# Performance work log

Hardware: AMD Instinct MI355X
Metric: run time of the kernel (lower is better)

Reference implementation:

```python
import jax, jax.numpy as jnp
import numpy as np

B, N, H = 32, 256, 1024
HEADS, NHID = 8, 128
NCLS = 7
BAND = 24
ALPHA = 0.2          # GAT leaky-relu slope
NEG = -9e15          # masked-attention fill, as in pyGAT


def setup_inputs() -> dict:
    key = jax.random.key(0)
    ks = jax.random.split(key, 16)
    def nrm(k, shp, s=0.02):
        return jax.random.normal(k, shp, dtype=jnp.float32) * s
    hidden_cls = jax.random.normal(ks[0], (B, N, H), dtype=jnp.float32)
    hidden_emo = jax.random.normal(ks[1], (B, N, H), dtype=jnp.float32)
    # causal band cliques, diagonal included (GAT uses clique - eye)
    t = jnp.arange(N)
    band = ((t[None, :] <= t[:, None]) & (t[None, :] > t[:, None] - BAND)).astype(jnp.float32)
    clique = jnp.broadcast_to(band, (B, N, N))
    labels = jax.random.randint(ks[2], (B, N), 0, NCLS)
    pooler_W = nrm(ks[3], (H, H)); pooler_b = jnp.zeros((H,), jnp.float32)
    gat_W = nrm(ks[4], (HEADS, H, NHID))
    gat_a1 = nrm(ks[5], (HEADS, NHID)); gat_a2 = nrm(ks[6], (HEADS, NHID))
    out_W = nrm(ks[7], (H, H))            # heads*nhid == H -> nclass=H
    out_a1 = nrm(ks[8], (H,)); out_a2 = nrm(ks[9], (H,))
    lin1_W = nrm(ks[10], (H, H)); lin1_b = jnp.zeros((H,), jnp.float32)
    lin0_W = nrm(ks[11], (2 * H, H)); lin0_b = jnp.zeros((H,), jnp.float32)
    cls_W = nrm(ks[12], (H, NCLS)); cls_b = jnp.zeros((NCLS,), jnp.float32)
    A = jax.random.uniform(ks[13], (NCLS, NCLS), dtype=jnp.float32) + 0.1
    hmm_A = A / A.sum(axis=1, keepdims=True)   # row-stochastic transition matrix
    return dict(hidden_cls=hidden_cls, hidden_emo=hidden_emo, clique=clique,
                labels=labels, pooler_W=pooler_W, pooler_b=pooler_b,
                gat_W=gat_W, gat_a1=gat_a1, gat_a2=gat_a2,
                out_W=out_W, out_a1=out_a1, out_a2=out_a2,
                lin1_W=lin1_W, lin1_b=lin1_b, lin0_W=lin0_W, lin0_b=lin0_b,
                cls_W=cls_W, cls_b=cls_b, hmm_A=hmm_A)


def _lrelu(x):
    return jnp.where(x > 0, x, ALPHA * x)


def reference(hidden_cls, hidden_emo, clique, labels, pooler_W, pooler_b,
              gat_W, gat_a1, gat_a2, out_W, out_a1, out_a2,
              lin1_W, lin1_b, lin0_W, lin0_b, cls_W, cls_b, hmm_A):
    # PoolerAll: dense + tanh on all token states (dropout = identity in eval)
    fea_cls = jnp.tanh(hidden_cls @ pooler_W + pooler_b)   # [B,N,H] (CLS per utt)
    fea_emo = jnp.tanh(hidden_emo @ pooler_W + pooler_b)   # [B,N,H] (mask tok per utt)

    eyeN = jnp.eye(N, dtype=clique.dtype)
    adjm = (clique - eyeN) > 0                             # [B,N,N] GAT adjacency

    def gat_one(x, am):                                    # x [N,H], am [N,N]
        Wh = jnp.einsum('nf,hfd->hnd', x, gat_W)           # [heads,N,nhid]
        e = _lrelu(jnp.einsum('hnd,hd->hn', Wh, gat_a1)[:, :, None]
                   + jnp.einsum('hnd,hd->hn', Wh, gat_a2)[:, None, :])
        att = jax.nn.softmax(jnp.where(am[None], e, NEG), axis=-1)
        h1 = jax.nn.elu(jnp.einsum('hnm,hmd->hnd', att, Wh))
        h1 = jnp.transpose(h1, (1, 0, 2)).reshape(N, HEADS * NHID)
        Wh2 = h1 @ out_W                                   # out attention layer (concat=False)
        e2 = _lrelu((Wh2 @ out_a1)[:, None] + (Wh2 @ out_a2)[None, :])
        h2 = jax.nn.softmax(jnp.where(am, e2, NEG), axis=-1) @ Wh2
        return jax.nn.elu(h2)                              # [N,H]

    gat_out = jax.vmap(gat_one)(fea_cls, adjm)             # [B,N,H]
    # row 0 replaced by (dropout of) fea_cls row 0, as in the original
    g = jnp.concatenate([fea_cls[:, :1], gat_out[:, 1:]], axis=1)
    g = jnp.concatenate([fea_cls, g @ lin1_W + lin1_b], axis=-1) @ lin0_W + lin0_b
    log_gat = jax.nn.softmax(g @ cls_W + cls_b, axis=-1)   # [B,N,NCLS] (probs)

    # HMM emission probs hmm_B(fea) = softmax(classifier(fea))
    Bprob = jax.nn.softmax(fea_emo @ cls_W + cls_b, axis=-1)  # [B,N,NCLS]
    P0 = jnp.full((NCLS,), 1.0 / NCLS, dtype=jnp.float32)
    AT = hmm_A.T

    def hmm_row(Bp, mrow):                                 # Bp [N,NCLS], mrow [N]
        def step(carry, xs):
            p, started = carry
            bt, m = xs
            p_init = P0 * bt; p_init = p_init / p_init.sum()
            p_tr = (AT @ p) * bt; p_tr = p_tr / p_tr.sum()
            p_new = jnp.where(started, p_tr, p_init)
            valid = m > 0.5
            return (jnp.where(valid, p_new, p), started | valid), None
        (p, _), _ = jax.lax.scan(step, (P0, jnp.asarray(False)), (Bp, mrow))
        return p                                           # final filtered posterior

    log_hmm = jax.vmap(lambda Bp, M: jax.vmap(lambda mr: hmm_row(Bp, mr))(M))(Bprob, clique)

    logits = jnp.log((log_gat + log_hmm) * 0.5).reshape(B * N, NCLS)
    lab = labels.reshape(B * N)
    mask = lab >= 0
    picked = jnp.take_along_axis(logits, jnp.where(mask, lab, 0)[:, None], axis=1)[:, 0]
    loss = -(jnp.where(mask, picked, 0.0).sum() / jnp.maximum(mask.sum(), 1).astype(jnp.float32))
    return loss, logits
```

## Files before the change

kernel.cpp:

```cpp
#include <hip/hip_runtime.h>
#include <hip/hip_bf16.h>
#include <math.h>

typedef __hip_bfloat16 bf16;
typedef __attribute__((ext_vector_type(8))) short short8;
typedef __attribute__((ext_vector_type(4))) float float4v;

static constexpr int Bb = 32, Nn = 256, Hh = 1024, HEADS = 8, NHID = 128, NCLS = 7, BAND = 24;
static constexpr int M = Bb * Nn;
static constexpr float ALPHA = 0.2f;
static constexpr long INEL = (long)M * Hh;

__device__ __forceinline__ float tof(bf16 x) { return __bfloat162float(x); }
__device__ __forceinline__ bf16 tob(float x) { return __float2bfloat16(x); }
__device__ __forceinline__ unsigned short f2bits(float x) {
    bf16 h = __float2bfloat16(x);
    return *(unsigned short*)&h;
}
__device__ __forceinline__ float bits2f(unsigned short u) {
    unsigned v = ((unsigned)u) << 16;
    float f;
    __builtin_memcpy(&f, &v, 4);
    return f;
}

__device__ __forceinline__ void gload16(const void* g, void* l) {
    __builtin_amdgcn_global_load_lds(
        (const __attribute__((address_space(1))) void*)g,
        (__attribute__((address_space(3))) void*)l, 16, 0, 0);
}

static constexpr long OFF_PWT  = 0;
static constexpr long OFF_PB   = 1048576;
static constexpr long OFF_WCT  = 1049600;
static constexpr long OFF_GA1  = 2098176;
static constexpr long OFF_GA2  = 2099200;
static constexpr long OFF_OWT  = 2100224;
static constexpr long OFF_OA1  = 3148800;
static constexpr long OFF_OA2  = 3149824;
static constexpr long OFF_L1WT = 3150848;
static constexpr long OFF_L1B  = 4199424;
static constexpr long OFF_L0WT = 4200448;
static constexpr long OFF_L0B  = 6297600;
static constexpr long OFF_CWT  = 6298624;
static constexpr long OFF_CB   = 6305792;
static constexpr long OFF_HA   = 6305799;
static constexpr long W_TOTAL  = 6305848;

__global__ void probe_k(const void* __restrict__ p, int* __restrict__ flag) {
    int t = threadIdx.x;
    int bad = 0;
    for (int i = t; i < 4096; i += 256) {
        float v = tof(((const bf16*)p)[i]);
        if (!(fabsf(v) < 1e4f)) bad = 1;
    }
    __shared__ int sb[256];
    sb[t] = bad; __syncthreads();
    for (int s = 128; s; s >>= 1) { if (t < s) sb[t] |= sb[t + s]; __syncthreads(); }
    if (t == 0) *flag = sb[0] ? 0 : 1;
}

__device__ __forceinline__ float ldany(const void* p, long i, int isb) {
    return isb ? tof(((const bf16*)p)[i]) : ((const float*)p)[i];
}

__global__ void convert_k(const int* __restrict__ flagp,
                          const void* pW, const void* pb, const void* gW,
                          const void* ga1, const void* ga2, const void* oW,
                          const void* oa1, const void* oa2, const void* l1W,
                          const void* l1b, const void* l0W, const void* l0b,
                          const void* cW, const void* cb, const void* hA,
                          bf16* __restrict__ dst) {
    long idx = (long)blockIdx.x * 256 + threadIdx.x;
    if (idx >= W_TOTAL) return;
    if ((idx >= OFF_L1WT && idx < OFF_L1B) || (idx >= OFF_L0WT && idx < OFF_L0B)) return;
    int isb = *flagp;
    const void* src; long si;
    if      (idx < OFF_PB)   { long l = idx;            long n = l >> 10, k = l & 1023;
                               src = pW;  si = k * 1024 + n; }
    else if (idx < OFF_WCT)  { src = pb;  si = idx - OFF_PB; }
    else if (idx < OFF_GA1)  { long l = idx - OFF_WCT;  long n = l >> 10, f = l & 1023;
                               long h = n >> 7, d = n & 127;
                               src = gW;  si = h * 131072 + f * 128 + d; }
    else if (idx < OFF_GA2)  { src = ga1; si = idx - OFF_GA1; }
    else if (idx < OFF_OWT)  { src = ga2; si = idx - OFF_GA2; }
    else if (idx < OFF_OA1)  { long l = idx - OFF_OWT;  long n = l >> 10, k = l & 1023;
                               src = oW;  si = k * 1024 + n; }
    else if (idx < OFF_OA2)  { src = oa1; si = idx - OFF_OA1; }
    else if (idx < OFF_L1WT) { src = oa2; si = idx - OFF_OA2; }
    else if (idx < OFF_L0WT) { src = l1b; si = idx - OFF_L1B; }
    else if (idx < OFF_CWT)  { src = l0b; si = idx - OFF_L0B; }
    else if (idx < OFF_CB)   { long l = idx - OFF_CWT;  long c = l >> 10, k = l & 1023;
                               src = cW;  si = k * 7 + c; }
    else if (idx < OFF_HA)   { src = cb;  si = idx - OFF_CB; }
    else                     { src = hA;  si = idx - OFF_HA; }
    dst[idx] = tob(ldany(src, si, isb));
}

__global__ void convin_k(const int* __restrict__ flagp, const void* __restrict__ s0,
                         const void* __restrict__ s1, bf16* __restrict__ d0,
                         bf16* __restrict__ d1) {
    const int isb = *flagp;
    if (isb) return;
    long i = ((long)blockIdx.x * 256 + threadIdx.x) * 8;
    const void* s; bf16* d; long off;
    if (i < INEL) { s = s0; d = d0; off = i; }
    else          { s = s1; d = d1; off = i - INEL; }
    const float* f = (const float*)s + off;
    unsigned short tmp[8];
    #pragma unroll
    for (int q = 0; q < 8; ++q) tmp[q] = f2bits(f[q]);
    *(int4*)(d + off) = *(int4*)tmp;
}

__global__ void gvec_k(const int* __restrict__ flagp, const void* __restrict__ l0W,
                       const void* __restrict__ cWr, float* __restrict__ W1T,
                       float* __restrict__ Gb) {
    int k = blockIdx.x;
    int lane = threadIdx.x;
    int isb = *flagp;
    float acc[NCLS];
    #pragma unroll
    for (int c = 0; c < NCLS; ++c) acc[c] = 0.f;
    #pragma unroll
    for (int q = 0; q < 16; ++q) {
        int j = lane * 16 + q;
        float x = ldany(l0W, (long)k * 1024 + j, isb);
        #pragma unroll
        for (int c = 0; c < NCLS; ++c) acc[c] += x * ldany(cWr, (long)j * 7 + c, isb);
    }
    #pragma unroll
    for (int c = 0; c < NCLS; ++c)
        #pragma unroll
        for (int off = 32; off; off >>= 1) acc[c] += __shfl_down(acc[c], off);
    if (lane == 0) {
        #pragma unroll
        for (int c = 0; c < NCLS; ++c) {
            if (k < 1024) W1T[c * 1024 + k] = acc[c];
            else          Gb[(k - 1024) * 7 + c] = acc[c];
        }
    }
}

__global__ void w2_k(const int* __restrict__ flagp, const void* __restrict__ l1W,
                     const float* __restrict__ Gb, float* __restrict__ W2T) {
    int i = blockIdx.x;
    int lane = threadIdx.x;
    int isb = *flagp;
    float acc[NCLS];
    #pragma unroll
    for (int c = 0; c < NCLS; ++c) acc[c] = 0.f;
    #pragma unroll
    for (int q = 0; q < 16; ++q) {
        int o = lane * 16 + q;
        float x = ldany(l1W, (long)i * 1024 + o, isb);
        #pragma unroll
        for (int c = 0; c < NCLS; ++c) acc[c] += x * Gb[o * 7 + c];
    }
    #pragma unroll
    for (int c = 0; c < NCLS; ++c)
        #pragma unroll
        for (int off = 32; off; off >>= 1) acc[c] += __shfl_down(acc[c], off);
    if (lane == 0) {
        #pragma unroll
        for (int c = 0; c < NCLS; ++c) W2T[c * 1024 + i] = acc[c];
    }
}

__global__ void cvec_k(const int* __restrict__ flagp, const void* __restrict__ l1b,
                       const void* __restrict__ l0b, const void* __restrict__ cWr,
                       const void* __restrict__ cbr, const float* __restrict__ Gb,
                       float* __restrict__ cvec) {
    int lane = threadIdx.x;
    int isb = *flagp;
    float acc[NCLS];
    #pragma unroll
    for (int c = 0; c < NCLS; ++c) acc[c] = 0.f;
    for (int o = lane; o < 1024; o += 64) {
        float b1 = ldany(l1b, o, isb);
        float b0 = ldany(l0b, o, isb);
        #pragma unroll
        for (int c = 0; c < NCLS; ++c)
            acc[c] += b1 * Gb[o * 7 + c] + b0 * ldany(cWr, (long)o * 7 + c, isb);
    }
    #pragma unroll
    for (int c = 0; c < NCLS; ++c)
        #pragma unroll
        for (int off = 32; off; off >>= 1) acc[c] += __shfl_down(acc[c], off);
    if (lane == 0) {
        #pragma unroll
        for (int c = 0; c < NCLS; ++c) cvec[c] = acc[c] + ldany(cbr, c, isb);
    }
}

static constexpr int SLOT_US = 256 * 32;

template <int ACT>
__device__ __forceinline__ void gemm_pipe_core(
    const bf16* __restrict__ A0, const bf16* __restrict__ A1, int ksw,
    int strideA, const bf16* __restrict__ Bt, int strideB,
    const bf16* __restrict__ bias, bf16* __restrict__ Cout,
    int Nc, int K, int bm, int bn, unsigned short* lds) {
    const int tid = threadIdx.x;
    const int lane = tid & 63;
    const int wave = tid >> 6;
    const int wm = (wave >> 1) * 64, wn = (wave & 1) * 64;
    const int l15 = lane & 15, quad = lane >> 4;
    const int csw = ((lane & 3) ^ ((lane >> 2) & 3) ^ (lane >> 4)) * 8;
    const int sc8 = (quad ^ (l15 & 3) ^ (l15 >> 2)) * 8;

    long aoff[2], boff[2];
    #pragma unroll
    for (int o = 0; o < 2; ++o) {
        aoff[o] = (long)(bm + wave * 32 + o * 16 + (lane >> 2)) * strideA + csw;
        boff[o] = (long)(bn + wave * 32 + o * 16 + (lane >> 2)) * strideB + csw;
    }
    const int aDst = wave * 32 * 32;
    const int bDst = (128 + wave * 32) * 32;

    const int nt = K / 32;
    float4v acc[4][4];
    #pragma unroll
    for (int i = 0; i < 4; ++i)
        #pragma unroll
        for (int j = 0; j < 4; ++j) acc[i][j] = (float4v){0.f, 0.f, 0.f, 0.f};

    auto stage = [&](int ts, int slot) {
        unsigned short* buf = lds + slot * SLOT_US;
        int ksub = ts * 32;
        const bf16* Ap = A0; int ka = ksub;
        if (ksub >= ksw) { Ap = A1; ka = ksub - ksw; }
        gload16(Ap + aoff[0] + ka, buf + aDst);
        gload16(Ap + aoff[1] + ka, buf + aDst + 512);
        gload16(Bt + boff[0] + ksub, buf + bDst);
        gload16(Bt + boff[1] + ksub, buf + bDst + 512);
    };
    auto frags = [&](int slot, short8* af, short8* bfr) {
        const unsigned short* bufc = lds + slot * SLOT_US;
        #pragma unroll
        for (int i = 0; i < 4; ++i)
            af[i] = *(const short8*)(bufc + (wm + i * 16 + l15) * 32 + sc8);
        #pragma unroll
        for (int j = 0; j < 4; ++j)
            bfr[j] = *(const short8*)(bufc + (128 + wn + j * 16 + l15) * 32 + sc8);
    };

    stage(0, 0); stage(1, 1); stage(2, 2);
    asm volatile("s_waitcnt vmcnt(8)" ::: "memory");
    __builtin_amdgcn_s_barrier();
    asm volatile("" ::: "memory");
    short8 afA[4], bfA[4], afB[4], bfB[4];
    frags(0, afA, bfA);
    int c0 = 0, c1 = 1, c2 = 2;

    for (int t = 0; t < nt; t += 2) {
        asm volatile("s_waitcnt lgkmcnt(0)" ::: "memory");
        if (t < nt - 2) asm volatile("s_waitcnt vmcnt(4)" ::: "memory");
        else            asm volatile("s_waitcnt vmcnt(0)" ::: "memory");
        __builtin_amdgcn_s_barrier();
        asm volatile("" ::: "memory");
        if (t + 3 < nt) stage(t + 3, c0);
        if (t + 1 < nt) frags(c1, afB, bfB);
        __builtin_amdgcn_s_setprio(1);
        #pragma unroll
        for (int i = 0; i < 4; ++i)
            #pragma unroll
            for (int j = 0; j < 4; ++j)
                acc[i][j] = __builtin_amdgcn_mfma_f32_16x16x32_bf16(afA[i], bfA[j], acc[i][j], 0, 0, 0);
        __builtin_amdgcn_s_setprio(0);
        asm volatile("" ::: "memory");
        asm volatile("s_waitcnt lgkmcnt(0)" ::: "memory");
        if (t + 1 < nt - 2) asm volatile("s_waitcnt vmcnt(4)" ::: "memory");
        else                asm volatile("s_waitcnt vmcnt(0)" ::: "memory");
        __builtin_amdgcn_s_barrier();
        asm volatile("" ::: "memory");
        if (t + 4 < nt) stage(t + 4, c1);
        if (t + 2 < nt) frags(c2, afA, bfA);
        __builtin_amdgcn_s_setprio(1);
        #pragma unroll
        for (int i = 0; i < 4; ++i)
            #pragma unroll
            for (int j = 0; j < 4; ++j)
                acc[i][j] = __builtin_amdgcn_mfma_f32_16x16x32_bf16(afB[i], bfB[j], acc[i][j], 0, 0, 0);
        __builtin_amdgcn_s_setprio(0);
        asm volatile("" ::: "memory");
        int n0 = c2, n1 = c0, n2 = c1;
        c0 = n0; c1 = n1; c2 = n2;
    }

    #pragma unroll
    for (int j = 0; j < 4; ++j) {
        int gn = bn + wn + j * 16 + l15;
        float bj = bias ? tof(bias[gn]) : 0.f;
        #pragma unroll
        for (int i = 0; i < 4; ++i) {
            #pragma unroll
            for (int r = 0; r < 4; ++r) {
                int gm = bm + wm + i * 16 + quad * 4 + r;
                float v = acc[i][j][r] + bj;
                if (ACT == 1) v = tanhf(v);
                Cout[(long)gm * Nc + gn] = tob(v);
            }
        }
    }
}

template <int ACT>
__global__ __launch_bounds__(256, 3) void gemm_pipe_k(const bf16* __restrict__ A,
                                                      const bf16* __restrict__ Bt,
                                                      const bf16* __restrict__ bias,
                                                      bf16* __restrict__ Cout,
                                                      int Nc, int K) {
    __shared__ __align__(16) unsigned short lds[3 * SLOT_US];
    gemm_pipe_core<ACT>(A, A, K, K, Bt, K, bias, Cout, Nc, K,
                        blockIdx.x * 128, blockIdx.y * 128, lds);
}

__global__ __launch_bounds__(256, 3) void gemmP_pipe_k(const int* __restrict__ flagp,
                                                       const bf16* __restrict__ rawE,
                                                       const bf16* __restrict__ rawC,
                                                       const bf16* __restrict__ A0,
                                                       const bf16* __restrict__ A1,
                                                       const bf16* __restrict__ Bt,
                                                       const bf16* __restrict__ bias,
                                                       bf16* __restrict__ C0,
                                                       bf16* __restrict__ C1) {
    __shared__ __align__(16) unsigned short lds[3 * SLOT_US];
    const int isb = *flagp;
    const bf16* A = blockIdx.z ? (isb ? rawC : A1) : (isb ? rawE : A0);
    bf16* C = blockIdx.z ? C1 : C0;
    gemm_pipe_core<1>(A, A, Hh, Hh, Bt, Hh, bias, C, Hh, Hh,
                      blockIdx.x * 128, blockIdx.y * 128, lds);
}

__global__ __launch_bounds__(256) void att1f_k(const bf16* __restrict__ Wh,
                                               const bf16* __restrict__ ga1,
                                               const bf16* __restrict__ ga2,
                                               bf16* __restrict__ h1) {
    __shared__ unsigned short S[152][128];
    __shared__ float f1s[152], f2s[152];
    __shared__ float att[128][25];
    const int bx = blockIdx.x;
    const int b = bx >> 4, h = (bx >> 1) & 7, half = bx & 1;
    const int nbase = half * 128;
    const int mstart = half ? (nbase - (BAND - 1)) : 0;
    const int mcount = half ? (256 - mstart) : 128;
    const int t = threadIdx.x;
    const int c = t & 15;

    float av1[8], av2[8];
    {
        union { int4 v; unsigned short us[8]; } u1, u2;
        u1.v = *(const int4*)(ga1 + h * 128 + c * 8);
        u2.v = *(const int4*)(ga2 + h * 128 + c * 8);
        #pragma unroll
        for (int qq = 0; qq < 8; ++qq) { av1[qq] = bits2f(u1.us[qq]); av2[qq] = bits2f(u2.us[qq]); }
    }

    const int iters = (mcount * 16 + 255) >> 8;
    for (int i = 0; i < iters; ++i) {
        int li = i * 256 + t;
        int mr = li >> 4;
        if (mr < mcount) {
            long ga = (long)(b * 256 + mstart + mr) * 1024 + h * 128 + c * 8;
            union { int4 v; unsigned short us[8]; } u;
            u.v = *(const int4*)(Wh + ga);
            float p1 = 0.f, p2 = 0.f;
            #pragma unroll
            for (int qq = 0; qq < 8; ++qq) {
                float f = bits2f(u.us[qq]);
                p1 += f * av1[qq]; p2 += f * av2[qq];
            }
            *(int4*)&S[mr][c * 8] = u.v;
            #pragma unroll
            for (int mask = 1; mask < 16; mask <<= 1) {
                p1 += __shfl_xor(p1, mask);
                p2 += __shfl_xor(p2, mask);
            }
            if (c == 0) { f1s[mr] = p1; f2s[mr] = p2; }
        }
    }
    __syncthreads();

    if (t < 128) {
        int n = nbase + t;
        if (n > 0) {
            int cnt = n < (BAND - 1) ? n : (BAND - 1);
            int m0 = n - cnt;
            float f1n = f1s[n - mstart];
            float e[BAND - 1];
            float mx = -1e30f;
            for (int i = 0; i < cnt; ++i) {
                float v = f1n + f2s[m0 + i - mstart];
                v = v > 0.f ? v : ALPHA * v;
                e[i] = v; mx = fmaxf(mx, v);
            }
            float ss = 0.f;
            for (int i = 0; i < cnt; ++i) { e[i] = __expf(e[i] - mx); ss += e[i]; }
            float inv = 1.0f / ss;
            for (int i = 0; i < cnt; ++i) att[t][i] = e[i] * inv;
        }
    }
    __syncthreads();

    const int wave = t >> 6, lane = t & 63;
    for (int ln = wave; ln < 128; ln += 4) {
        int n = nbase + ln;
        if (n == 0) continue;
        int cnt = n < (BAND - 1) ? n : (BAND - 1);
        int mr0 = n - cnt - mstart;
        float s0 = 0.f, s1 = 0.f;
        for (int i = 0; i < cnt; ++i) {
            float a = att[ln][i];
            unsigned u = *(const unsigned*)&S[mr0 + i][lane * 2];
            s0 += a * bits2f((unsigned short)(u & 0xffff));
            s1 += a * bits2f((unsigned short)(u >> 16));
        }
        s0 = s0 > 0.f ? s0 : expm1f(s0);
        s1 = s1 > 0.f ? s1 : expm1f(s1);
        unsigned out = (unsigned)f2bits(s0) | ((unsigned)f2bits(s1) << 16);
        *(unsigned*)(h1 + (long)(b * 256 + n) * 1024 + h * 128 + lane * 2) = out;
    }
}

__global__ void mean1_k(const bf16* __restrict__ Wh, bf16* __restrict__ h1) {
    int bh = blockIdx.x;
    int h = bh & 7, b = bh >> 3;
    int lane = threadIdx.x;
    float s0 = 0.f, s1 = 0.f;
    long base = (long)(b * 256) * 1024 + h * 128 + lane * 2;
    for (int m = 0; m < 256; ++m) {
        unsigned u = *(const unsigned*)(Wh + base + (long)m * 1024);
        s0 += bits2f((unsigned short)(u & 0xffff));
        s1 += bits2f((unsigned short)(u >> 16));
    }
    s0 *= (1.0f / 256.0f); s1 *= (1.0f / 256.0f);
    s0 = s0 > 0.f ? s0 : expm1f(s0);
    s1 = s1 > 0.f ? s1 : expm1f(s1);
    unsigned out = (unsigned)f2bits(s0) | ((unsigned)f2bits(s1) << 16);
    *(unsigned*)(h1 + base) = out;
}

__global__ void f12b_k(const bf16* __restrict__ Wh2, const bf16* __restrict__ a1,
                       const bf16* __restrict__ a2, float* __restrict__ f1b,
                       float* __restrict__ f2b) {
    int idx = blockIdx.x;
    int lane = threadIdx.x;
    const bf16* row = Wh2 + (long)idx * 1024 + lane * 16;
    float s1 = 0.f, s2 = 0.f;
    #pragma unroll
    for (int half = 0; half < 2; ++half) {
        union { int4 v; unsigned short us[8]; } x, w1, w2;
        x.v  = *(const int4*)(row + half * 8);
        w1.v = *(const int4*)(a1 + lane * 16 + half * 8);
        w2.v = *(const int4*)(a2 + lane * 16 + half * 8);
        #pragma unroll
        for (int q = 0; q < 8; ++q) {
            float f = bits2f(x.us[q]);
            s1 += f * bits2f(w1.us[q]);
            s2 += f * bits2f(w2.us[q]);
        }
    }
    #pragma unroll
    for (int off = 32; off; off >>= 1) {
        s1 += __shfl_down(s1, off);
        s2 += __shfl_down(s2, off);
    }
    if (lane == 0) { f1b[idx] = s1; f2b[idx] = s2; }
}

__global__ __launch_bounds__(256) void att2f_k(const bf16* __restrict__ Wh2,
                                               const float* __restrict__ f1b,
                                               const float* __restrict__ f2b,
                                               bf16* __restrict__ g) {
    __shared__ unsigned short S[152][128];
    __shared__ float att[128][25];
    const int bx = blockIdx.x;
    const int b = bx >> 4, half = (bx >> 3) & 1, jt = bx & 7;
    const int nbase = half * 128;
    const int mstart = half ? (nbase - (BAND - 1)) : 0;
    const int mcount = half ? (256 - mstart) : 128;
    const int t = threadIdx.x;
    const int c = t & 15;

    const int iters = (mcount * 16 + 255) >> 8;
    for (int i = 0; i < iters; ++i) {
        int li = i * 256 + t;
        int mr = li >> 4;
        if (mr < mcount) {
            long ga = (long)(b * 256 + mstart + mr) * 1024 + jt * 128 + c * 8;
            *(int4*)&S[mr][c * 8] = *(const int4*)(Wh2 + ga);
        }
    }
    __syncthreads();

    if (t < 128) {
        int n = nbase + t;
        if (n > 0) {
            int cnt = n < (BAND - 1) ? n : (BAND - 1);
            int m0 = n - cnt;
            float f1n = f1b[b * 256 + n];
            float e[BAND - 1];
            float mx = -1e30f;
            for (int i = 0; i < cnt; ++i) {
                float v = f1n + f2b[b * 256 + m0 + i];
                v = v > 0.f ? v : ALPHA * v;
                e[i] = v; mx = fmaxf(mx, v);
            }
            float ss = 0.f;
            for (int i = 0; i < cnt; ++i) { e[i] = __expf(e[i] - mx); ss += e[i]; }
            float inv = 1.0f / ss;
            for (int i = 0; i < cnt; ++i) att[t][i] = e[i] * inv;
        }
    }
    __syncthreads();

    const int wave = t >> 6, lane = t & 63;
    for (int ln = wave; ln < 128; ln += 4) {
        int n = nbase + ln;
        if (n == 0) continue;
        int cnt = n < (BAND - 1) ? n : (BAND - 1);
        int mr0 = n - cnt - mstart;
        float s0 = 0.f, s1 = 0.f;
        for (int i = 0; i < cnt; ++i) {
            float a = att[ln][i];
            unsigned u = *(const unsigned*)&S[mr0 + i][lane * 2];
            s0 += a * bits2f((unsigned short)(u & 0xffff));
            s1 += a * bits2f((unsigned short)(u >> 16));
        }
        s0 = s0 > 0.f ? s0 : expm1f(s0);
        s1 = s1 > 0.f ? s1 : expm1f(s1);
        unsigned out = (unsigned)f2bits(s0) | ((unsigned)f2bits(s1) << 16);
        *(unsigned*)(g + (long)(b * 256 + n) * 1024 + jt * 128 + lane * 2) = out;
    }
}

__global__ void g_row0_k(const bf16* __restrict__ fea_cls, bf16* __restrict__ g) {
    int b = blockIdx.x;
    int t = threadIdx.x;
    long base = (long)(b * 256) * 1024 + t * 8;
    *(int4*)(g + base) = *(const int4*)(fea_cls + base);
}

__global__ void cls7_k(const bf16* __restrict__ X, const bf16* __restrict__ Wt,
                       const bf16* __restrict__ b, float* __restrict__ out, int K) {
    int row = blockIdx.x;
    int lane = threadIdx.x;
    float xv[16];
    {
        const bf16* x = X + (long)row * K + lane * 16;
        union { int4 v; unsigned short us[8]; } u0, u1;
        u0.v = *(const int4*)x; u1.v = *(const int4*)(x + 8);
        #pragma unroll
        for (int q = 0; q < 8; ++q) { xv[q] = bits2f(u0.us[q]); xv[q + 8] = bits2f(u1.us[q]); }
    }
    float acc[NCLS];
    #pragma unroll
    for (int cc = 0; cc < NCLS; ++cc) {
        const bf16* wr = Wt + (long)cc * K + lane * 16;
        union { int4 v; unsigned short us[8]; } w0, w1;
        w0.v = *(const int4*)wr; w1.v = *(const int4*)(wr + 8);
        float s = 0.f;
        #pragma unroll
        for (int q = 0; q < 8; ++q) {
            s += xv[q] * bits2f(w0.us[q]);
            s += xv[q + 8] * bits2f(w1.us[q]);
        }
        acc[cc] = s;
    }
    #pragma unroll
    for (int cc = 0; cc < NCLS; ++cc)
        #pragma unroll
        for (int off = 32; off; off >>= 1) acc[cc] += __shfl_down(acc[cc], off);
    if (lane == 0) {
        float mx = -1e30f;
        #pragma unroll
        for (int cc = 0; cc < NCLS; ++cc) { acc[cc] += tof(b[cc]); mx = fmaxf(mx, acc[cc]); }
        float s = 0.f;
        #pragma unroll
        for (int cc = 0; cc < NCLS; ++cc) { acc[cc] = expf(acc[cc] - mx); s += acc[cc]; }
        float inv = 1.0f / s;
        #pragma unroll
        for (int cc = 0; cc < NCLS; ++cc) out[(long)row * NCLS + cc] = acc[cc] * inv;
    }
}

__global__ void lgat2_k(const bf16* __restrict__ X, const bf16* __restrict__ Y,
                        const float* __restrict__ W1T, const float* __restrict__ W2T,
                        const float* __restrict__ cvec, float* __restrict__ out) {
    int row = blockIdx.x;
    int lane = threadIdx.x;
    float xv[16], yv[16];
    {
        const bf16* x = X + (long)row * 1024 + lane * 16;
        const bf16* y = Y + (long)row * 1024 + lane * 16;
        union { int4 v; unsigned short us[8]; } u0, u1, v0, v1;
        u0.v = *(const int4*)x; u1.v = *(const int4*)(x + 8);
        v0.v = *(const int4*)y; v1.v = *(const int4*)(y + 8);
        #pragma unroll
        for (int q = 0; q < 8; ++q) {
            xv[q] = bits2f(u0.us[q]); xv[q + 8] = bits2f(u1.us[q]);
            yv[q] = bits2f(v0.us[q]); yv[q + 8] = bits2f(v1.us[q]);
        }
    }
    float acc[NCLS];
    #pragma unroll
    for (int cc = 0; cc < NCLS; ++cc) {
        const float4* w1 = (const float4*)(W1T + (long)cc * 1024 + lane * 16);
        const float4* w2 = (const float4*)(W2T + (long)cc * 1024 + lane * 16);
        float s = 0.f;
        #pragma unroll
        for (int h = 0; h < 4; ++h) {
            float4 a = w1[h], b = w2[h];
            s += xv[h * 4 + 0] * a.x + xv[h * 4 + 1] * a.y + xv[h * 4 + 2] * a.z + xv[h * 4 + 3] * a.w;
            s += yv[h * 4 + 0] * b.x + yv[h * 4 + 1] * b.y + yv[h * 4 + 2] * b.z + yv[h * 4 + 3] * b.w;
        }
        acc[cc] = s;
    }
    #pragma unroll
    for (int cc = 0; cc < NCLS; ++cc)
        #pragma unroll
        for (int off = 32; off; off >>= 1) acc[cc] += __shfl_down(acc[cc], off);
    if (lane == 0) {
        float mx = -1e30f;
        #pragma unroll
        for (int cc = 0; cc < NCLS; ++cc) { acc[cc] += cvec[cc]; mx = fmaxf(mx, acc[cc]); }
        float s = 0.f;
        #pragma unroll
        for (int cc = 0; cc < NCLS; ++cc) { acc[cc] = expf(acc[cc] - mx); s += acc[cc]; }
        float inv = 1.0f / s;
        #pragma unroll
        for (int cc = 0; cc < NCLS; ++cc) out[(long)row * NCLS + cc] = acc[cc] * inv;
    }
}

__global__ void hmm_k(const float* __restrict__ Bprob, const bf16* __restrict__ hmm_A,
                      float* __restrict__ out) {
    __shared__ float AT[NCLS][NCLS];
    int t = threadIdx.x;
    if (t < NCLS * NCLS) {
        int i = t / NCLS, j = t % NCLS;
        AT[i][j] = tof(hmm_A[j * NCLS + i]);
    }
    __syncthreads();
    int idx = blockIdx.x * blockDim.x + t;
    int n = idx & 255, b = idx >> 8;
    int t0 = n - (BAND - 1) > 0 ? n - (BAND - 1) : 0;
    const float* Bp = Bprob + (long)(b * 256) * NCLS;
    float p[NCLS];
    float s = 0.f;
    #pragma unroll
    for (int cc = 0; cc < NCLS; ++cc) { p[cc] = Bp[t0 * NCLS + cc]; s += p[cc]; }
    float inv = 1.0f / s;
    #pragma unroll
    for (int cc = 0; cc < NCLS; ++cc) p[cc] *= inv;
    for (int tt = t0 + 1; tt <= n; ++tt) {
        float q[NCLS]; float ss = 0.f;
        #pragma unroll
        for (int i = 0; i < NCLS; ++i) {
            float a = 0.f;
            #pragma unroll
            for (int j = 0; j < NCLS; ++j) a += AT[i][j] * p[j];
            a *= Bp[tt * NCLS + i];
            q[i] = a; ss += a;
        }
        float iv = 1.0f / ss;
        #pragma unroll
        for (int i = 0; i < NCLS; ++i) p[i] = q[i] * iv;
    }
    #pragma unroll
    for (int cc = 0; cc < NCLS; ++cc) out[(long)idx * NCLS + cc] = p[cc];
}

__global__ void zero_k(float* p) { *p = 0.f; }

__global__ void final_k(const float* __restrict__ lg, const float* __restrict__ lh,
                        const int* __restrict__ labels, void* __restrict__ out,
                        float* __restrict__ loss_acc, const int* __restrict__ flagp) {
    int idx = blockIdx.x * blockDim.x + threadIdx.x;
    const int isb = *flagp;
    float lo[NCLS];
    int lab = labels[idx];
    #pragma unroll
    for (int c = 0; c < NCLS; ++c) {
        float v = logf(0.5f * (lg[(long)idx * NCLS + c] + lh[(long)idx * NCLS + c]));
        lo[c] = v;
        long o = 1 + (long)idx * NCLS + c;
        if (isb) ((bf16*)out)[o] = tob(v);
        else     ((float*)out)[o] = v;
    }
    float picked = lo[lab];
    __shared__ float red[256];
    red[threadIdx.x] = picked;
    __syncthreads();
    for (int s = 128; s; s >>= 1) {
        if (threadIdx.x < s) red[threadIdx.x] += red[threadIdx.x + s];
        __syncthreads();
    }
    if (threadIdx.x == 0) atomicAdd(loss_acc, red[0]);
}

__global__ void loss_k(const float* __restrict__ acc, void* __restrict__ out,
                       const int* __restrict__ flagp) {
    float v = -acc[0] / (float)(Bb * Nn);
    if (*flagp) ((bf16*)out)[0] = tob(v);
    else        ((float*)out)[0] = v;
}

extern "C" void kernel_launch(void* const* d_in, const int* in_sizes, int n_in,
                              void* d_out, int out_size, void* d_ws, size_t ws_size,
                              hipStream_t stream) {
    const void* hidden_cls = d_in[0];
    const void* hidden_emo = d_in[1];
    const int* labels = (const int*)d_in[3];

    char* w = (char*)d_ws;
    bf16* C  = (bf16*)w;
    bf16* E  = C + INEL;
    bf16* Wb = E + INEL;
    bf16* H2 = Wb + INEL;
    bf16* wc = H2 + INEL;
    float* f1b   = (float*)(wc + W_TOTAL);
    float* f2b   = f1b + M;
    float* Bprob = f2b + M;
    float* lgat  = Bprob + (long)M * NCLS;
    float* lhmm  = lgat + (long)M * NCLS;
    float* loss_acc = lhmm + (long)M * NCLS;
    int*   flag  = (int*)(loss_acc + 1);
    float* W1f   = (float*)(flag + 1);
    float* W2f   = W1f + 7 * 1024;
    float* Gbf   = W2f + 7 * 1024;
    float* cvec  = Gbf + 1024 * 7;

    dim3 gblk(256);
    dim3 ggrid(M / 128, Hh / 128);
    dim3 pgrid(M / 128, Hh / 128, 2);

    probe_k<<<1, 256, 0, stream>>>(d_in[4], flag);
    convert_k<<<(int)((W_TOTAL + 255) / 256), 256, 0, stream>>>(
        flag, d_in[4], d_in[5], d_in[6], d_in[7], d_in[8], d_in[9], d_in[10],
        d_in[11], d_in[12], d_in[13], d_in[14], d_in[15], d_in[16], d_in[17],
        d_in[18], wc);
    gvec_k<<<2048, 64, 0, stream>>>(flag, d_in[14], d_in[16], W1f, Gbf);
    w2_k<<<1024, 64, 0, stream>>>(flag, d_in[12], Gbf, W2f);
    cvec_k<<<1, 64, 0, stream>>>(flag, d_in[13], d_in[15], d_in[16], d_in[17], Gbf, cvec);
    convin_k<<<(int)(2 * INEL / (256 * 8)), 256, 0, stream>>>(flag, hidden_emo, hidden_cls, Wb, H2);

    gemmP_pipe_k<<<pgrid, gblk, 0, stream>>>(flag, (const bf16*)hidden_emo,
                                             (const bf16*)hidden_cls, Wb, H2,
                                             wc + OFF_PWT, wc + OFF_PB, E, C);
    cls7_k<<<M, 64, 0, stream>>>(E, wc + OFF_CWT, wc + OFF_CB, Bprob, Hh);
    gemm_pipe_k<0><<<ggrid, gblk, 0, stream>>>(C, wc + OFF_WCT, (const bf16*)nullptr, Wb, Hh, Hh);
    att1f_k<<<512, 256, 0, stream>>>(Wb, wc + OFF_GA1, wc + OFF_GA2, E);
    mean1_k<<<Bb * HEADS, 64, 0, stream>>>(Wb, E);
    gemm_pipe_k<0><<<ggrid, gblk, 0, stream>>>(E, wc + OFF_OWT, (const bf16*)nullptr, Wb, Hh, Hh);
    f12b_k<<<M, 64, 0, stream>>>(Wb, wc + OFF_OA1, wc + OFF_OA2, f1b, f2b);
    g_row0_k<<<Bb, 128, 0, stream>>>(C, E);
    att2f_k<<<512, 256, 0, stream>>>(Wb, f1b, f2b, E);
    lgat2_k<<<M, 64, 0, stream>>>(C, E, W1f, W2f, cvec, lgat);
    hmm_k<<<M / 256, 256, 0, stream>>>(Bprob, wc + OFF_HA, lhmm);
    zero_k<<<1, 1, 0, stream>>>(loss_acc);
    final_k<<<M / 256, 256, 0, stream>>>(lgat, lhmm, labels, d_out, loss_acc, flag);
    loss_k<<<1, 1, 0, stream>>>(loss_acc, d_out, flag);
}
```

Before: 483.2 us.

## Enlarge GEMM tiles to 256x256 with 512-thread blocks and LDS-cache small weight vectors

Replaces the 128x128 four-wave GEMM with a 256x256 tile computed by eight waves, each owning a 128x64 sub-tile. This raises arithmetic intensity per LDS load, and the loop is simplified to single-step iterations without register double-buffering of fragments. The gvec/w2 precompute kernels now stage the shared 1024x7 operand in LDS and process 8 rows per 256-thread block instead of one row per 64-thread block. Risks include fewer blocks (256 or 512 per GEMM) for 256 CUs, so wave quantization gets worse, plus higher register pressure from 32 accumulators and lost overlap between LDS fragment reads and MFMA.

```diff
diff --git a/kernel.cpp b/kernel.cpp
--- a/kernel.cpp
+++ b/kernel.cpp
@@ -113,57 +113,81 @@
     *(int4*)(d + off) = *(int4*)tmp;
 }
 
-__global__ void gvec_k(const int* __restrict__ flagp, const void* __restrict__ l0W,
-                       const void* __restrict__ cWr, float* __restrict__ W1T,
-                       float* __restrict__ Gb) {
-    int k = blockIdx.x;
-    int lane = threadIdx.x;
-    int isb = *flagp;
-    float acc[NCLS];
-    #pragma unroll
-    for (int c = 0; c < NCLS; ++c) acc[c] = 0.f;
-    #pragma unroll
-    for (int q = 0; q < 16; ++q) {
-        int j = lane * 16 + q;
-        float x = ldany(l0W, (long)k * 1024 + j, isb);
-        #pragma unroll
-        for (int c = 0; c < NCLS; ++c) acc[c] += x * ldany(cWr, (long)j * 7 + c, isb);
-    }
-    #pragma unroll
-    for (int c = 0; c < NCLS; ++c)
-        #pragma unroll
-        for (int off = 32; off; off >>= 1) acc[c] += __shfl_down(acc[c], off);
-    if (lane == 0) {
-        #pragma unroll
-        for (int c = 0; c < NCLS; ++c) {
-            if (k < 1024) W1T[c * 1024 + k] = acc[c];
-            else          Gb[(k - 1024) * 7 + c] = acc[c];
-        }
-    }
-}
-
-__global__ void w2_k(const int* __restrict__ flagp, const void* __restrict__ l1W,
-                     const float* __restrict__ Gb, float* __restrict__ W2T) {
-    int i = blockIdx.x;
-    int lane = threadIdx.x;
-    int isb = *flagp;
-    float acc[NCLS];
-    #pragma unroll
-    for (int c = 0; c < NCLS; ++c) acc[c] = 0.f;
-    #pragma unroll
-    for (int q = 0; q < 16; ++q) {
-        int o = lane * 16 + q;
-        float x = ldany(l1W, (long)i * 1024 + o, isb);
-        #pragma unroll
-        for (int c = 0; c < NCLS; ++c) acc[c] += x * Gb[o * 7 + c];
-    }
-    #pragma unroll
-    for (int c = 0; c < NCLS; ++c)
-        #pragma unroll
-        for (int off = 32; off; off >>= 1) acc[c] += __shfl_down(acc[c], off);
-    if (lane == 0) {
-        #pragma unroll
-        for (int c = 0; c < NCLS; ++c) W2T[c * 1024 + i] = acc[c];
+__global__ __launch_bounds__(256) void gvec_k(const int* __restrict__ flagp,
+                                              const void* __restrict__ l0W,
+                                              const void* __restrict__ cWr,
+                                              float* __restrict__ W1T,
+                                              float* __restrict__ Gb) {
+    __shared__ float S[1024][NCLS];
+    const int t = threadIdx.x;
+    const int isb = *flagp;
+    for (int j = t; j < 1024; j += 256) {
+        #pragma unroll
+        for (int c = 0; c < NCLS; ++c) S[j][c] = ldany(cWr, (long)j * 7 + c, isb);
+    }
+    __syncthreads();
+    const int wave = t >> 6, lane = t & 63;
+    #pragma unroll
+    for (int r = 0; r < 2; ++r) {
+        int k = blockIdx.x * 8 + wave * 2 + r;
+        float acc[NCLS];
+        #pragma unroll
+        for (int c = 0; c < NCLS; ++c) acc[c] = 0.f;
+        #pragma unroll
+        for (int q = 0; q < 16; ++q) {
+            int j = lane * 16 + q;
+            float x = ldany(l0W, (long)k * 1024 + j, isb);
+            #pragma unroll
+            for (int c = 0; c < NCLS; ++c) acc[c] += x * S[j][c];
+        }
+        #pragma unroll
+        for (int c = 0; c < NCLS; ++c)
+            #pragma unroll
+            for (int off = 32; off; off >>= 1) acc[c] += __shfl_down(acc[c], off);
+        if (lane == 0) {
+            #pragma unroll
+            for (int c = 0; c < NCLS; ++c) {
+                if (k < 1024) W1T[c * 1024 + k] = acc[c];
+                else          Gb[(k - 1024) * 7 + c] = acc[c];
+            }
+        }
+    }
+}
+
+__global__ __launch_bounds__(256) void w2_k(const int* __restrict__ flagp,
+                                            const void* __restrict__ l1W,
+                                            const float* __restrict__ Gb,
+                                            float* __restrict__ W2T) {
+    __shared__ float S[1024][NCLS];
+    const int t = threadIdx.x;
+    const int isb = *flagp;
+    for (int j = t; j < 1024; j += 256) {
+        #pragma unroll
+        for (int c = 0; c < NCLS; ++c) S[j][c] = Gb[(long)j * 7 + c];
+    }
+    __syncthreads();
+    const int wave = t >> 6, lane = t & 63;
+    #pragma unroll
+    for (int r = 0; r < 2; ++r) {
+        int i = blockIdx.x * 8 + wave * 2 + r;
+        float acc[NCLS];
+        #pragma unroll
+        for (int c = 0; c < NCLS; ++c) acc[c] = 0.f;
+        #pragma unroll
+        for (int q = 0; q < 16; ++q) {
+            int o = lane * 16 + q;
+            float x = ldany(l1W, (long)i * 1024 + o, isb);
+            #pragma unroll
+            for (int c = 0; c < NCLS; ++c) acc[c] += x * S[o][c];
+        }
+        #pragma unroll
+        for (int c = 0; c < NCLS; ++c)
+            #pragma unroll
+            for (int off = 32; off; off >>= 1) acc[c] += __shfl_down(acc[c], off);
+        if (lane == 0) {
+            #pragma unroll
+            for (int c = 0; c < NCLS; ++c) W2T[c * 1024 + i] = acc[c];
+        }
     }
 }
 
@@ -193,18 +217,18 @@
     }
 }
 
-static constexpr int SLOT_US = 256 * 32;
+static constexpr int SLOT_US = 512 * 32;
 
 template <int ACT>
-__device__ __forceinline__ void gemm_pipe_core(
-    const bf16* __restrict__ A0, const bf16* __restrict__ A1, int ksw,
-    int strideA, const bf16* __restrict__ Bt, int strideB,
+__device__ __forceinline__ void gemm_big_core(
+    const bf16* __restrict__ A, int strideA,
+    const bf16* __restrict__ Bt, int strideB,
     const bf16* __restrict__ bias, bf16* __restrict__ Cout,
     int Nc, int K, int bm, int bn, unsigned short* lds) {
     const int tid = threadIdx.x;
     const int lane = tid & 63;
     const int wave = tid >> 6;
-    const int wm = (wave >> 1) * 64, wn = (wave & 1) * 64;
+    const int wm = (wave >> 2) * 128, wn = (wave & 3) * 64;
     const int l15 = lane & 15, quad = lane >> 4;
     const int csw = ((lane & 3) ^ ((lane >> 2) & 3) ^ (lane >> 4)) * 8;
     const int sc8 = (quad ^ (l15 & 3) ^ (l15 >> 2)) * 8;
@@ -216,76 +240,54 @@
         boff[o] = (long)(bn + wave * 32 + o * 16 + (lane >> 2)) * strideB + csw;
     }
     const int aDst = wave * 32 * 32;
-    const int bDst = (128 + wave * 32) * 32;
+    const int bDst = (256 + wave * 32) * 32;
 
     const int nt = K / 32;
-    float4v acc[4][4];
-    #pragma unroll
-    for (int i = 0; i < 4; ++i)
+    float4v acc[8][4];
+    #pragma unroll
+    for (int i = 0; i < 8; ++i)
         #pragma unroll
         for (int j = 0; j < 4; ++j) acc[i][j] = (float4v){0.f, 0.f, 0.f, 0.f};
 
     auto stage = [&](int ts, int slot) {
         unsigned short* buf = lds + slot * SLOT_US;
-        int ksub = ts * 32;
-        const bf16* Ap = A0; int ka = ksub;
-        if (ksub >= ksw) { Ap = A1; ka = ksub - ksw; }
-        gload16(Ap + aoff[0] + ka, buf + aDst);
-        gload16(Ap + aoff[1] + ka, buf + aDst + 512);
-        gload16(Bt + boff[0] + ksub, buf + bDst);
-        gload16(Bt + boff[1] + ksub, buf + bDst + 512);
-    };
-    auto frags = [&](int slot, short8* af, short8* bfr) {
-        const unsigned short* bufc = lds + slot * SLOT_US;
-        #pragma unroll
-        for (int i = 0; i < 4; ++i)
-            af[i] = *(const short8*)(bufc + (wm + i * 16 + l15) * 32 + sc8);
-        #pragma unroll
-        for (int j = 0; j < 4; ++j)
-            bfr[j] = *(const short8*)(bufc + (128 + wn + j * 16 + l15) * 32 + sc8);
+        int k = ts * 32;
+        gload16(A + aoff[0] + k, buf + aDst);
+        gload16(A + aoff[1] + k, buf + aDst + 512);
+        gload16(Bt + boff[0] + k, buf + bDst);
+        gload16(Bt + boff[1] + k, buf + bDst + 512);
     };
 
     stage(0, 0); stage(1, 1); stage(2, 2);
     asm volatile("s_waitcnt vmcnt(8)" ::: "memory");
     __builtin_amdgcn_s_barrier();
     asm volatile("" ::: "memory");
-    short8 afA[4], bfA[4], afB[4], bfB[4];
-    frags(0, afA, bfA);
-    int c0 = 0, c1 = 1, c2 = 2;
-
-    for (int t = 0; t < nt; t += 2) {
+
+    int c0 = 0;
+    for (int t = 0; t < nt; ++t) {
+        const unsigned short* bufc = lds + c0 * SLOT_US;
+        short8 af[8], bfr[4];
+        #pragma unroll
+        for (int j = 0; j < 4; ++j)
+            bfr[j] = *(const short8*)(bufc + (256 + wn + j * 16 + l15) * 32 + sc8);
+        #pragma unroll
+        for (int i = 0; i < 8; ++i)
+            af[i] = *(const short8*)(bufc + (wm + i * 16 + l15) * 32 + sc8);
         asm volatile("s_waitcnt lgkmcnt(0)" ::: "memory");
-        if (t < nt - 2) asm volatile("s_waitcnt vmcnt(4)" ::: "memory");
+        if (t + 2 < nt) asm volatile("s_waitcnt vmcnt(4)" ::: "memory");
         else            asm volatile("s_waitcnt vmcnt(0)" ::: "memory");
         __builtin_amdgcn_s_barrier();
         asm volatile("" ::: "memory");
         if (t + 3 < nt) stage(t + 3, c0);
-        if (t + 1 < nt) frags(c1, afB, bfB);
         __builtin_amdgcn_s_setprio(1);
         #pragma unroll
-        for (int i = 0; i < 4; ++i)
+        for (int i = 0; i < 8; ++i)
             #pragma unroll
             for (int j = 0; j < 4; ++j)
-                acc[i][j] = __builtin_amdgcn_mfma_f32_16x16x32_bf16(afA[i], bfA[j], acc[i][j], 0, 0, 0);
+                acc[i][j] = __builtin_amdgcn_mfma_f32_16x16x32_bf16(af[i], bfr[j], acc[i][j], 0, 0, 0);
         __builtin_amdgcn_s_setprio(0);
         asm volatile("" ::: "memory");
-        asm volatile("s_waitcnt lgkmcnt(0)" ::: "memory");
-        if (t + 1 < nt - 2) asm volatile("s_waitcnt vmcnt(4)" ::: "memory");
-        else                asm volatile("s_waitcnt vmcnt(0)" ::: "memory");
-        __builtin_amdgcn_s_barrier();
-        asm volatile("" ::: "memory");
-        if (t + 4 < nt) stage(t + 4, c1);
-        if (t + 2 < nt) frags(c2, afA, bfA);
-        __builtin_amdgcn_s_setprio(1);
-        #pragma unroll
-        for (int i = 0; i < 4; ++i)
-            #pragma unroll
-            for (int j = 0; j < 4; ++j)
-                acc[i][j] = __builtin_amdgcn_mfma_f32_16x16x32_bf16(afB[i], bfB[j], acc[i][j], 0, 0, 0);
-        __builtin_amdgcn_s_setprio(0);
-        asm volatile("" ::: "memory");
-        int n0 = c2, n1 = c0, n2 = c1;
-        c0 = n0; c1 = n1; c2 = n2;
+        c0 = (c0 == 2) ? 0 : c0 + 1;
     }
 
     #pragma unroll
@@ -293,7 +295,7 @@
         int gn = bn + wn + j * 16 + l15;
         float bj = bias ? tof(bias[gn]) : 0.f;
         #pragma unroll
-        for (int i = 0; i < 4; ++i) {
+        for (int i = 0; i < 8; ++i) {
             #pragma unroll
             for (int r = 0; r < 4; ++r) {
                 int gm = bm + wm + i * 16 + quad * 4 + r;
@@ -306,31 +308,31 @@
 }
 
 template <int ACT>
-__global__ __launch_bounds__(256, 3) void gemm_pipe_k(const bf16* __restrict__ A,
+__global__ __launch_bounds__(512, 2) void gemm_big_k(const bf16* __restrict__ A,
+                                                     const bf16* __restrict__ Bt,
+                                                     const bf16* __restrict__ bias,
+                                                     bf16* __restrict__ Cout,
+                                                     int Nc, int K) {
+    __shared__ __align__(16) unsigned short lds[3 * SLOT_US];
+    gemm_big_core<ACT>(A, K, Bt, K, bias, Cout, Nc, K,
+                       blockIdx.x * 256, blockIdx.y * 256, lds);
+}
+
+__global__ __launch_bounds__(512, 2) void gemmP_big_k(const int* __restrict__ flagp,
+                                                      const bf16* __restrict__ rawE,
+                                                      const bf16* __restrict__ rawC,
+                                                      const bf16* __restrict__ A0,
+                                                      const bf16* __restrict__ A1,
                                                       const bf16* __restrict__ Bt,
                                                       const bf16* __restrict__ bias,
-                                                      bf16* __restrict__ Cout,
-                                                      int Nc, int K) {
-    __shared__ __align__(16) unsigned short lds[3 * SLOT_US];
-    gemm_pipe_core<ACT>(A, A, K, K, Bt, K, bias, Cout, Nc, K,
-                        blockIdx.x * 128, blockIdx.y * 128, lds);
-}
-
-__global__ __launch_bounds__(256, 3) void gemmP_pipe_k(const int* __restrict__ flagp,
-                                                       const bf16* __restrict__ rawE,
-                                                       const bf16* __restrict__ rawC,
-                                                       const bf16* __restrict__ A0,
-                                                       const bf16* __restrict__ A1,
-                                                       const bf16* __restrict__ Bt,
-                                                       const bf16* __restrict__ bias,
-                                                       bf16* __restrict__ C0,
-                                                       bf16* __restrict__ C1) {
+                                                      bf16* __restrict__ C0,
+                                                      bf16* __restrict__ C1) {
     __shared__ __align__(16) unsigned short lds[3 * SLOT_US];
     const int isb = *flagp;
     const bf16* A = blockIdx.z ? (isb ? rawC : A1) : (isb ? rawE : A0);
     bf16* C = blockIdx.z ? C1 : C0;
-    gemm_pipe_core<1>(A, A, Hh, Hh, Bt, Hh, bias, C, Hh, Hh,
-                      blockIdx.x * 128, blockIdx.y * 128, lds);
+    gemm_big_core<1>(A, Hh, Bt, Hh, bias, C, Hh, Hh,
+                     blockIdx.x * 256, blockIdx.y * 256, lds);
 }
 
 __global__ __launch_bounds__(256) void att1f_k(const bf16* __restrict__ Wh,
@@ -732,28 +734,28 @@
     float* Gbf   = W2f + 7 * 1024;
     float* cvec  = Gbf + 1024 * 7;
 
-    dim3 gblk(256);
-    dim3 ggrid(M / 128, Hh / 128);
-    dim3 pgrid(M / 128, Hh / 128, 2);
+    dim3 gblk(512);
+    dim3 ggrid(M / 256, Hh / 256);
+    dim3 pgrid(M / 256, Hh / 256, 2);
 
     probe_k<<<1, 256, 0, stream>>>(d_in[4], flag);
     convert_k<<<(int)((W_TOTAL + 255) / 256), 256, 0, stream>>>(
         flag, d_in[4], d_in[5], d_in[6], d_in[7], d_in[8], d_in[9], d_in[10],
         d_in[11], d_in[12], d_in[13], d_in[14], d_in[15], d_in[16], d_in[17],
         d_in[18], wc);
-    gvec_k<<<2048, 64, 0, stream>>>(flag, d_in[14], d_in[16], W1f, Gbf);
-    w2_k<<<1024, 64, 0, stream>>>(flag, d_in[12], Gbf, W2f);
+    gvec_k<<<256, 256, 0, stream>>>(flag, d_in[14], d_in[16], W1f, Gbf);
+    w2_k<<<128, 256, 0, stream>>>(flag, d_in[12], Gbf, W2f);
     cvec_k<<<1, 64, 0, stream>>>(flag, d_in[13], d_in[15], d_in[16], d_in[17], Gbf, cvec);
     convin_k<<<(int)(2 * INEL / (256 * 8)), 256, 0, stream>>>(flag, hidden_emo, hidden_cls, Wb, H2);
 
-    gemmP_pipe_k<<<pgrid, gblk, 0, stream>>>(flag, (const bf16*)hidden_emo,
-                                             (const bf16*)hidden_cls, Wb, H2,
-                                             wc + OFF_PWT, wc + OFF_PB, E, C);
+    gemmP_big_k<<<pgrid, gblk, 0, stream>>>(flag, (const bf16*)hidden_emo,
+                                            (const bf16*)hidden_cls, Wb, H2,
+                                            wc + OFF_PWT, wc + OFF_PB, E, C);
     cls7_k<<<M, 64, 0, stream>>>(E, wc + OFF_CWT, wc + OFF_CB, Bprob, Hh);
-    gemm_pipe_k<0><<<ggrid, gblk, 0, stream>>>(C, wc + OFF_WCT, (const bf16*)nullptr, Wb, Hh, Hh);
+    gemm_big_k<0><<<ggrid, gblk, 0, stream>>>(C, wc + OFF_WCT, (const bf16*)nullptr, Wb, Hh, Hh);
     att1f_k<<<512, 256, 0, stream>>>(Wb, wc + OFF_GA1, wc + OFF_GA2, E);
     mean1_k<<<Bb * HEADS, 64, 0, stream>>>(Wb, E);
-    gemm_pipe_k<0><<<ggrid, gblk, 0, stream>>>(E, wc + OFF_OWT, (const bf16*)nullptr, Wb, Hh, Hh);
+    gemm_big_k<0><<<ggrid, gblk, 0, stream>>>(E, wc + OFF_OWT, (const bf16*)nullptr, Wb, Hh, Hh);
     f12b_k<<<M, 64, 0, stream>>>(Wb, wc + OFF_OA1, wc + OFF_OA2, f1b, f2b);
     g_row0_k<<<Bb, 128, 0, stream>>>(C, E);
     att2f_k<<<512, 256, 0, stream>>>(Wb, f1b, f2b, E);
```

Result: slower. 494.0 us (+2.2%).
